# Kernel tuning notes

Hardware: AMD Instinct MI355X
Metric: run time of the kernel (lower is better)

Reference implementation:

```python
import jax, jax.numpy as jnp
import numpy as np

NBITS = 4
DIM = 768
HEADS = 12
HEAD_DIM = DIM // HEADS
B, N = 8, 1024
SCALE = HEAD_DIM ** -0.5


def round_ste(x):
    # round_pass: straight-through round
    return x + jax.lax.stop_gradient(jnp.round(x) - x)


def grad_scale(x, g):
    # forward: x, backward: grad * g
    return x * g + jax.lax.stop_gradient(x * (1.0 - g))


def actq(x, alpha, zp, signed):
    # ActQ eval-mode forward: per-channel alpha/zero_point collapsed via .mean()
    if signed:
        Qn, Qp = -2 ** (NBITS - 1), 2 ** (NBITS - 1) - 1
    else:
        Qn, Qp = 0, 2 ** NBITS - 1
    a = jnp.mean(alpha)
    z = jnp.mean(round_ste(zp))
    xq = round_ste(jnp.clip(x / a + z, Qn, Qp))
    return (xq - z) * a


def linearq(x, w, b, alpha_w, act_alpha, act_zp):
    # LSQ weight quant (per-out-channel alpha with grad_scale) + input ActQ
    Qn, Qp = -2 ** (NBITS - 1), 2 ** (NBITS - 1) - 1
    g = 1.0 / np.sqrt(w.size * Qp)
    a = grad_scale(alpha_w, g)[:, None]  # [out,1]
    w_q = round_ste(jnp.clip(w / a, Qn, Qp)) * a
    xq = actq(x, act_alpha, act_zp, signed=True)
    y = jnp.einsum('...i,oi->...o', xq, w_q)
    return y if b is None else y + b


def layernorm(x, g, b, eps=1e-5):
    m = jnp.mean(x, axis=-1, keepdims=True)
    v = jnp.var(x, axis=-1, keepdims=True)  # biased, matches torch LayerNorm
    return (x - m) / jnp.sqrt(v + eps) * g + b


def setup_inputs() -> dict:
    key = jax.random.key(0)
    ks = jax.random.split(key, 20)
    u = lambda k, shape: jax.random.uniform(k, shape, jnp.float32, 0.01, 0.05)
    zp = lambda k, shape: jax.random.uniform(k, shape, jnp.float32, -0.3, 0.3)
    return {
        'x0': jax.random.normal(ks[0], (B, N, DIM), jnp.float32),
        'qkv_w': jax.random.normal(ks[1], (3 * DIM, DIM), jnp.float32) * 0.02,
        'qkv_alpha_w': u(ks[2], (3 * DIM,)),
        'qkv_act_alpha': u(ks[3], (DIM,)),
        'qkv_act_zp': zp(ks[4], (DIM,)),
        'norm_q_g': jnp.ones((HEAD_DIM,), jnp.float32),
        'norm_q_b': jnp.zeros((HEAD_DIM,), jnp.float32),
        'norm_k_g': jnp.ones((HEAD_DIM,), jnp.float32),
        'norm_k_b': jnp.zeros((HEAD_DIM,), jnp.float32),
        'q_alpha': u(ks[5], (HEADS,)), 'q_zp': zp(ks[6], (HEADS,)),
        'k_alpha': u(ks[7], (HEADS,)), 'k_zp': zp(ks[8], (HEADS,)),
        'v_alpha': u(ks[9], (HEADS,)), 'v_zp': zp(ks[10], (HEADS,)),
        'attn_alpha': u(ks[11], (HEADS,)), 'attn_zp': zp(ks[12], (HEADS,)),
        'proj_w': jax.random.normal(ks[13], (DIM, DIM), jnp.float32) * 0.02,
        'proj_b': jnp.zeros((DIM,), jnp.float32),
        'proj_alpha_w': u(ks[14], (DIM,)),
        'proj_act_alpha': u(ks[15], (DIM,)),
        'proj_act_zp': zp(ks[16], (DIM,)),
    }


def reference(x0, qkv_w, qkv_alpha_w, qkv_act_alpha, qkv_act_zp,
              norm_q_g, norm_q_b, norm_k_g, norm_k_b,
              q_alpha, q_zp, k_alpha, k_zp, v_alpha, v_zp,
              attn_alpha, attn_zp,
              proj_w, proj_b, proj_alpha_w, proj_act_alpha, proj_act_zp):
    b, n, c = x0.shape
    qkv = linearq(x0, qkv_w, None, qkv_alpha_w, qkv_act_alpha, qkv_act_zp)
    qkv = qkv.reshape(b, n, 3, HEADS, HEAD_DIM).transpose(2, 0, 3, 1, 4)  # [3,B,H,N,hd]
    q0, k0, v0 = qkv[0], qkv[1], qkv[2]
    q1 = layernorm(q0, norm_q_g, norm_q_b)
    k1 = layernorm(k0, norm_k_g, norm_k_b)
    q2 = actq(q1, q_alpha, q_zp, signed=True)
    k2 = actq(k1, k_alpha, k_zp, signed=True)
    v2 = actq(v0, v_alpha, v_zp, signed=True)
    attn = jax.nn.softmax(jnp.einsum('bhqd,bhkd->bhqk', q2, k2) * SCALE, axis=-1)
    attn = actq(attn, attn_alpha, attn_zp, signed=False)  # softmax output is unsigned
    x1 = jnp.einsum('bhqk,bhkd->bhqd', attn, v2).transpose(0, 2, 1, 3).reshape(b, n, c)
    return linearq(x1, proj_w, proj_b, proj_alpha_w, proj_act_alpha, proj_act_zp)
```

## Files before the change

### kernel.cpp

```cpp
#include <hip/hip_runtime.h>
#include <hip/hip_bf16.h>

#define HEADS 12
#define HD 64
#define DIM 768
#define SEQ 1024
#define NTOK 8192
#define TRIPLE 2304
#define BHTOT 96

typedef __attribute__((ext_vector_type(8))) short bf16x8;
typedef __attribute__((ext_vector_type(4))) float f32x4;
typedef __attribute__((ext_vector_type(4))) int i32x4;

#define MFMA_B16(a, b, c) __builtin_amdgcn_mfma_f32_16x16x32_bf16((a), (b), (c), 0, 0, 0)
#define MFMA_I8(a, b, c) __builtin_amdgcn_mfma_i32_16x16x64_i8((a), (b), (c), 0, 0, 0)

__device__ __forceinline__ unsigned short f2bf(float f) {
  unsigned int u = __float_as_uint(f);
  unsigned int r = (u + 0x7fffu + ((u >> 16) & 1u)) >> 16;
  return (unsigned short)r;
}
__device__ __forceinline__ float qclamp(float v, float lo, float hi) {
  return fminf(fmaxf(v, lo), hi);
}

__device__ float block_mean(const float* p, int n, int rnd, float* red) {
  int t = threadIdx.x;
  float s = 0.f;
  for (int i = t; i < n; i += 256) { float v = p[i]; s += rnd ? rintf(v) : v; }
  red[t] = s;
  __syncthreads();
  for (int o = 128; o > 0; o >>= 1) { if (t < o) red[t] += red[t + o]; __syncthreads(); }
  float m = red[0] / (float)n;
  __syncthreads();
  return m;
}

__global__ __launch_bounds__(256) void k_prep(
    const float* qaa, const float* qzp, const float* qa, const float* qz,
    const float* ka, const float* kz, const float* va, const float* vz,
    const float* ata, const float* atz, const float* pa, const float* pz,
    float* sc) {
  __shared__ float red[256];
  float r0 = block_mean(qaa, 768, 0, red);
  float r1 = block_mean(qzp, 768, 1, red);
  float r2 = block_mean(qa, 12, 0, red);
  float r3 = block_mean(qz, 12, 1, red);
  float r4 = block_mean(ka, 12, 0, red);
  float r5 = block_mean(kz, 12, 1, red);
  float r6 = block_mean(va, 12, 0, red);
  float r7 = block_mean(vz, 12, 1, red);
  float r8 = block_mean(ata, 12, 0, red);
  float r9 = block_mean(atz, 12, 1, red);
  float r10 = block_mean(pa, 768, 0, red);
  float r11 = block_mean(pz, 768, 1, red);
  if (threadIdx.x == 0) {
    sc[0] = r0; sc[1] = r1; sc[2] = r2; sc[3] = r3; sc[4] = r4; sc[5] = r5;
    sc[6] = r6; sc[7] = r7; sc[8] = r8; sc[9] = r9; sc[10] = r10; sc[11] = r11;
  }
}

__global__ __launch_bounds__(256) void k_quant_act(
    const float* __restrict__ x, signed char* __restrict__ xq,
    const float* __restrict__ sc, int n) {
  int i = (blockIdx.x * 256 + threadIdx.x) * 4;
  if (i >= n) return;
  float a = sc[0], z = sc[1];
  float4 v = *(const float4*)(x + i);
  int b0 = (int)rintf(qclamp(v.x / a + z, -8.f, 7.f));
  int b1 = (int)rintf(qclamp(v.y / a + z, -8.f, 7.f));
  int b2 = (int)rintf(qclamp(v.z / a + z, -8.f, 7.f));
  int b3 = (int)rintf(qclamp(v.w / a + z, -8.f, 7.f));
  ((int*)xq)[i >> 2] = (b0 & 255) | ((b1 & 255) << 8) | ((b2 & 255) << 16) | (b3 << 24);
}

__global__ __launch_bounds__(256) void k_quant_w(
    const float* __restrict__ w, const float* __restrict__ alpha,
    signed char* __restrict__ wq, int n, int K) {
  int i = (blockIdx.x * 256 + threadIdx.x) * 4;
  if (i >= n) return;
  float a = alpha[i / K];
  float4 v = *(const float4*)(w + i);
  int b0 = (int)rintf(qclamp(v.x / a, -8.f, 7.f));
  int b1 = (int)rintf(qclamp(v.y / a, -8.f, 7.f));
  int b2 = (int)rintf(qclamp(v.z / a, -8.f, 7.f));
  int b3 = (int)rintf(qclamp(v.w / a, -8.f, 7.f));
  ((int*)wq)[i >> 2] = (b0 & 255) | ((b1 & 255) << 8) | ((b2 & 255) << 16) | (b3 << 24);
}

__global__ __launch_bounds__(256) void k_wsum(
    const signed char* __restrict__ wq, float* __restrict__ s, int K) {
  const int w = threadIdx.x >> 6, l = threadIdx.x & 63;
  const int row = blockIdx.x * 4 + w;
  const int* rp = (const int*)(wq + (size_t)row * K);
  int acc = 0;
  for (int idx = l; idx < K / 4; idx += 64) {
    int u = rp[idx];
    acc += (int)(signed char)u + (int)(signed char)(u >> 8) +
           (int)(signed char)(u >> 16) + (int)(signed char)(u >> 24);
  }
#pragma unroll
  for (int off = 32; off > 0; off >>= 1) acc += __shfl_xor(acc, off);
  if (l == 0) s[row] = (float)acc;
}

__device__ __forceinline__ void stage_i8(
    const signed char* __restrict__ g, int ldk,
    signed char* lds, int wv, int l) {
#pragma unroll
  for (int j = 0; j < 4; ++j) {
    __builtin_amdgcn_global_load_lds(
        (const __attribute__((address_space(1))) void*)(
            g + (size_t)(wv * 32 + j * 8 + (l >> 3)) * ldk + (l & 7) * 16),
        (__attribute__((address_space(3))) void*)(lds + wv * 4096 + j * 1024),
        16, 0, 0);
  }
}
__device__ __forceinline__ void stage_i8_64(
    const signed char* __restrict__ g, int ldk,
    signed char* lds, int wv, int l) {
#pragma unroll
  for (int j = 0; j < 2; ++j) {
    __builtin_amdgcn_global_load_lds(
        (const __attribute__((address_space(1))) void*)(
            g + (size_t)(wv * 16 + j * 8 + (l >> 3)) * ldk + (l & 7) * 16),
        (__attribute__((address_space(3))) void*)(lds + wv * 2048 + j * 1024),
        16, 0, 0);
  }
}

__global__ __launch_bounds__(256) void k_gemm_qkv(
    const signed char* __restrict__ A, const signed char* __restrict__ Bw,
    const float* __restrict__ colscale, const float* __restrict__ wsum,
    const float* __restrict__ sc,
    const float* __restrict__ nqg, const float* __restrict__ nqb,
    const float* __restrict__ nkg, const float* __restrict__ nkb,
    unsigned short* __restrict__ q2b, unsigned short* __restrict__ k2b,
    unsigned short* __restrict__ v2t) {
  __shared__ __align__(16) char smem[65536];
  signed char (*As)[16384] = (signed char(*)[16384])smem;
  signed char (*Bs)[16384] = (signed char(*)[16384])(smem + 32768);
  unsigned short (*T)[132] = (unsigned short(*)[132])smem;
  const int t = threadIdx.x;
  const int brow = blockIdx.x * 128, bcol = blockIdx.y * 128;
  const int w = t >> 6, l = t & 63;
  const int lr = l & 15, lg = l >> 4;
  const int wr = (w >> 1) * 64, wc = (w & 1) * 64;
  i32x4 acc[4][4] = {};

  auto compute = [&](const signed char* sa, const signed char* sb) {
#pragma unroll
    for (int ks = 0; ks < 2; ++ks) {
      i32x4 af[4], bfr[4];
#pragma unroll
      for (int i = 0; i < 4; ++i) {
        af[i] = *(const i32x4*)&sa[(wr + i * 16 + lr) * 128 + ks * 64 + lg * 16];
        bfr[i] = *(const i32x4*)&sb[(wc + i * 16 + lr) * 128 + ks * 64 + lg * 16];
      }
#pragma unroll
      for (int i = 0; i < 4; ++i)
#pragma unroll
        for (int j = 0; j < 4; ++j)
          acc[i][j] = MFMA_I8(af[i], bfr[j], acc[i][j]);
    }
  };

  const int nt = DIM / 128;
  stage_i8(A + (size_t)brow * DIM, DIM, As[0], w, l);
  stage_i8(Bw + (size_t)bcol * DIM, DIM, Bs[0], w, l);
  __syncthreads();
  int cur = 0;
  for (int kt = 0; kt < nt - 1; ++kt) {
    stage_i8(A + (size_t)brow * DIM + (kt + 1) * 128, DIM, As[cur ^ 1], w, l);
    stage_i8(Bw + (size_t)bcol * DIM + (kt + 1) * 128, DIM, Bs[cur ^ 1], w, l);
    compute(As[cur], Bs[cur]);
    __syncthreads();
    cur ^= 1;
  }
  compute(As[cur], Bs[cur]);

  const float sact = sc[0], zin = sc[1];
  float s_j[4], zw_j[4];
#pragma unroll
  for (int j = 0; j < 4; ++j) {
    const int col = bcol + wc + j * 16 + lr;
    s_j[j] = sact * colscale[col];
    zw_j[j] = zin * wsum[col];
  }
  f32x4 fac[4][4];
#pragma unroll
  for (int i = 0; i < 4; ++i)
#pragma unroll
    for (int j = 0; j < 4; ++j)
#pragma unroll
      for (int r = 0; r < 4; ++r)
        fac[i][j][r] = ((float)acc[i][j][r] - zw_j[j]) * s_j[j];

  const int seg = bcol / DIM;
  const int h0 = ((bcol % DIM) + wc) / 64;
  if (seg < 2) {
    const float* gp = seg ? nkg : nqg;
    const float* bp = seg ? nkb : nqb;
    const float aq_ = seg ? sc[4] : sc[2];
    const float zq_ = seg ? sc[5] : sc[3];
    float gj[4], bj[4];
#pragma unroll
    for (int j = 0; j < 4; ++j) { gj[j] = gp[j * 16 + lr]; bj[j] = bp[j * 16 + lr]; }
    unsigned short* dstb = seg ? k2b : q2b;
#pragma unroll
    for (int i = 0; i < 4; ++i)
#pragma unroll
      for (int r = 0; r < 4; ++r) {
        float sum = fac[i][0][r] + fac[i][1][r] + fac[i][2][r] + fac[i][3][r];
        sum += __shfl_xor(sum, 1); sum += __shfl_xor(sum, 2);
        sum += __shfl_xor(sum, 4); sum += __shfl_xor(sum, 8);
        float m = sum * (1.0f / 64.0f);
        float vs = 0.f;
#pragma unroll
        for (int j = 0; j < 4; ++j) { float d = fac[i][j][r] - m; vs += d * d; }
        vs += __shfl_xor(vs, 1); vs += __shfl_xor(vs, 2);
        vs += __shfl_xor(vs, 4); vs += __shfl_xor(vs, 8);
        float inv = 1.0f / sqrtf(vs * (1.0f / 64.0f) + 1e-5f);
        int row = brow + wr + i * 16 + lg * 4 + r;
        int b_ = row >> 10, n_ = row & (SEQ - 1);
        unsigned short* dst = dstb + (((size_t)(b_ * HEADS + h0) << 10) + n_) * HD;
#pragma unroll
        for (int j = 0; j < 4; ++j) {
          float yv = (fac[i][j][r] - m) * inv * gj[j] + bj[j];
          float qv = rintf(qclamp(yv / aq_ + zq_, -8.f, 7.f)) - zq_;
          dst[j * 16 + lr] = f2bf(qv);
        }
      }
  } else {
    const float av_ = sc[6], zv = sc[7];
    __syncthreads();
#pragma unroll
    for (int i = 0; i < 4; ++i)
#pragma unroll
      for (int r = 0; r < 4; ++r) {
        const int rowl = wr + i * 16 + lg * 4 + r;
#pragma unroll
        for (int j = 0; j < 4; ++j) {
          float qv = rintf(qclamp(fac[i][j][r] / av_ + zv, -8.f, 7.f)) - zv;
          T[wc + j * 16 + lr][rowl] = f2bf(qv);
        }
      }
    __syncthreads();
    const int b_ = brow >> 10, n0 = brow & (SEQ - 1);
    const int hbase = (bcol % DIM) / 64;
#pragma unroll
    for (int it = 0; it < 32; ++it) {
      const int dcol = w * 32 + it;
      const int h_ = hbase + (dcol >> 6);
      const int d_ = dcol & 63;
      unsigned int val = *(const unsigned int*)&T[dcol][2 * l];
      *(unsigned int*)(v2t + ((size_t)(b_ * HEADS + h_) << 16) +
                       (size_t)d_ * SEQ + n0 + 2 * l) = val;
    }
  }
}

__global__ __launch_bounds__(256) void k_gemm(
    const signed char* __restrict__ A, const signed char* __restrict__ Bw,
    float* __restrict__ out, const float* __restrict__ colscale,
    const float* __restrict__ wsum, const float* __restrict__ bias,
    const float* __restrict__ sc, int sact_idx, int zin_idx,
    int M, int Nt, int K) {
  __shared__ signed char As[2][64 * 128];
  __shared__ signed char Bs[2][128 * 128];
  const int t = threadIdx.x;
  const int brow = blockIdx.x * 64, bcol = blockIdx.y * 128;
  const int w = t >> 6, l = t & 63;
  const int lr = l & 15, lg = l >> 4;
  const int wr = (w >> 1) * 32, wc = (w & 1) * 64;
  i32x4 acc[2][4] = {};

  auto compute = [&](const signed char* sa, const signed char* sb) {
#pragma unroll
    for (int ks = 0; ks < 2; ++ks) {
      i32x4 af[2], bfr[4];
#pragma unroll
      for (int i = 0; i < 2; ++i)
        af[i] = *(const i32x4*)&sa[(wr + i * 16 + lr) * 128 + ks * 64 + lg * 16];
#pragma unroll
      for (int j = 0; j < 4; ++j)
        bfr[j] = *(const i32x4*)&sb[(wc + j * 16 + lr) * 128 + ks * 64 + lg * 16];
#pragma unroll
      for (int i = 0; i < 2; ++i)
#pragma unroll
        for (int j = 0; j < 4; ++j)
          acc[i][j] = MFMA_I8(af[i], bfr[j], acc[i][j]);
    }
  };

  const int nt = K / 128;
  stage_i8_64(A + (size_t)brow * K, K, As[0], w, l);
  stage_i8(Bw + (size_t)bcol * K, K, Bs[0], w, l);
  __syncthreads();
  int cur = 0;
  for (int kt = 0; kt < nt - 1; ++kt) {
    stage_i8_64(A + (size_t)brow * K + (kt + 1) * 128, K, As[cur ^ 1], w, l);
    stage_i8(Bw + (size_t)bcol * K + (kt + 1) * 128, K, Bs[cur ^ 1], w, l);
    compute(As[cur], Bs[cur]);
    __syncthreads();
    cur ^= 1;
  }
  compute(As[cur], Bs[cur]);

  const float sact = sc[sact_idx], zin = sc[zin_idx];
#pragma unroll
  for (int j = 0; j < 4; ++j) {
    const int col = bcol + wc + j * 16 + lr;
    const float s = sact * colscale[col];
    const float zw = zin * wsum[col];
    const float bb = bias ? bias[col] : 0.f;
#pragma unroll
    for (int i = 0; i < 2; ++i) {
      const int row0 = brow + wr + i * 16 + lg * 4;
#pragma unroll
      for (int r = 0; r < 4; ++r)
        out[(size_t)(row0 + r) * Nt + col] = ((float)acc[i][j][r] - zw) * s + bb;
    }
  }
}

__global__ __launch_bounds__(256, 3) void k_attn(
    const unsigned short* __restrict__ q2b, const unsigned short* __restrict__ k2b,
    const unsigned short* __restrict__ v2t, signed char* __restrict__ x1q,
    const float* __restrict__ sc) {
  __shared__ unsigned short Ks[128][72];
  __shared__ unsigned short Vs[64][136];
  __shared__ unsigned short Ps[4][32][40];
  const int t = threadIdx.x;
  const int w = t >> 6, l = t & 63;
  const int lr = l & 15, lg = l >> 4;
  const int bid = (int)(blockIdx.x & 7) * 96 + (int)(blockIdx.x >> 3);
  const int bh = bid >> 3, qc = bid & 7;
  const unsigned short* Qg = q2b + (size_t)bh * (SEQ * HD);
  const unsigned short* Kg = k2b + (size_t)bh * (SEQ * HD);
  const unsigned short* Vg = v2t + (size_t)bh * (SEQ * HD);
  const float aq = sc[2], ak = sc[4], av_ = sc[6], aa = sc[8], za = sc[9];
  const float ap = sc[10], zpp = sc[11];
  const float sqk2 = aq * ak * 0.125f * 1.44269504f;
  const float spv = aa * av_;
  const int qr0 = qc * 128 + w * 32;

  bf16x8 qf[2][2];
#pragma unroll
  for (int rt = 0; rt < 2; ++rt)
#pragma unroll
    for (int ks = 0; ks < 2; ++ks)
      qf[rt][ks] = *(const bf16x8*)(Qg + (size_t)(qr0 + rt * 16 + lr) * HD + ks * 32 + lg * 8);

  const int sr = t >> 1, sc0 = (t & 1) * 32;
  const int vr = t >> 2, vc0 = (t & 3) * 32;

  float lacc[2][4] = {};
  for (int kt = 0; kt < SEQ; kt += 128) {
    const uint4* g = (const uint4*)(Kg + (size_t)(kt + sr) * HD + sc0);
    uint4 u0 = g[0], u1 = g[1], u2 = g[2], u3 = g[3];
    __syncthreads();
    { uint4* d = (uint4*)&Ks[sr][sc0]; d[0] = u0; d[1] = u1; d[2] = u2; d[3] = u3; }
    __syncthreads();
#pragma unroll
    for (int ct = 0; ct < 8; ++ct) {
      const int kl = ct * 16 + lr;
      bf16x8 kf0 = *(const bf16x8*)&Ks[kl][lg * 8];
      bf16x8 kf1 = *(const bf16x8*)&Ks[kl][32 + lg * 8];
#pragma unroll
      for (int rt = 0; rt < 2; ++rt) {
        f32x4 s4 = {0.f, 0.f, 0.f, 0.f};
        s4 = MFMA_B16(qf[rt][0], kf0, s4);
        s4 = MFMA_B16(qf[rt][1], kf1, s4);
#pragma unroll
        for (int r = 0; r < 4; ++r)
          lacc[rt][r] += __builtin_amdgcn_exp2f(s4[r] * sqk2);
      }
    }
  }
#pragma unroll
  for (int off = 1; off < 16; off <<= 1)
#pragma unroll
    for (int rt = 0; rt < 2; ++rt)
#pragma unroll
      for (int r = 0; r < 4; ++r) lacc[rt][r] += __shfl_xor(lacc[rt][r], off);
  float pinv[2][4];
#pragma unroll
  for (int rt = 0; rt < 2; ++rt)
#pragma unroll
    for (int r = 0; r < 4; ++r) pinv[rt][r] = 1.0f / (lacc[rt][r] * aa);

  f32x4 oacc[2][4] = {};
  for (int kt = 0; kt < SEQ; kt += 128) {
    const uint4* gk = (const uint4*)(Kg + (size_t)(kt + sr) * HD + sc0);
    uint4 u0 = gk[0], u1 = gk[1], u2 = gk[2], u3 = gk[3];
    const uint4* gv = (const uint4*)(Vg + (size_t)vr * SEQ + kt + vc0);
    uint4 w0 = gv[0], w1 = gv[1], w2 = gv[2], w3 = gv[3];
    __syncthreads();
    { uint4* d = (uint4*)&Ks[sr][sc0]; d[0] = u0; d[1] = u1; d[2] = u2; d[3] = u3; }
    { uint4* d = (uint4*)&Vs[vr][vc0]; d[0] = w0; d[1] = w1; d[2] = w2; d[3] = w3; }
    __syncthreads();
#pragma unroll
    for (int q4 = 0; q4 < 4; ++q4) {
#pragma unroll
      for (int c2 = 0; c2 < 2; ++c2) {
        const int ct = q4 * 2 + c2;
        const int kl = ct * 16 + lr;
        bf16x8 kf0 = *(const bf16x8*)&Ks[kl][lg * 8];
        bf16x8 kf1 = *(const bf16x8*)&Ks[kl][32 + lg * 8];
#pragma unroll
        for (int rt = 0; rt < 2; ++rt) {
          f32x4 s4 = {0.f, 0.f, 0.f, 0.f};
          s4 = MFMA_B16(qf[rt][0], kf0, s4);
          s4 = MFMA_B16(qf[rt][1], kf1, s4);
#pragma unroll
          for (int r = 0; r < 4; ++r) {
            float e = __builtin_amdgcn_exp2f(s4[r] * sqk2);
            float p = fmaf(e, pinv[rt][r], za);
            float qv = rintf(qclamp(p, 0.f, 15.f)) - za;
            Ps[w][rt * 16 + lg * 4 + r][c2 * 16 + lr] = f2bf(qv);
          }
        }
      }
      bf16x8 vf[4], pf[2];
#pragma unroll
      for (int dt = 0; dt < 4; ++dt)
        vf[dt] = *(const bf16x8*)&Vs[dt * 16 + lr][q4 * 32 + lg * 8];
#pragma unroll
      for (int rt = 0; rt < 2; ++rt)
        pf[rt] = *(const bf16x8*)&Ps[w][rt * 16 + lr][lg * 8];
#pragma unroll
      for (int rt = 0; rt < 2; ++rt)
#pragma unroll
        for (int dt = 0; dt < 4; ++dt)
          oacc[rt][dt] = MFMA_B16(pf[rt], vf[dt], oacc[rt][dt]);
    }
  }
  const int b_ = bh / HEADS, h_ = bh % HEADS;
#pragma unroll
  for (int rt = 0; rt < 2; ++rt)
#pragma unroll
    for (int dt = 0; dt < 4; ++dt) {
      const int col = h_ * HD + dt * 16 + lr;
#pragma unroll
      for (int r = 0; r < 4; ++r) {
        const int qrow = qr0 + rt * 16 + lg * 4 + r;
        float x1v = oacc[rt][dt][r] * spv;
        int xi = (int)rintf(qclamp(x1v / ap + zpp, -8.f, 7.f));
        x1q[(size_t)(b_ * SEQ + qrow) * DIM + col] = (signed char)xi;
      }
    }
}

extern "C" void kernel_launch(void* const* d_in, const int* in_sizes, int n_in,
                              void* d_out, int out_size, void* d_ws, size_t ws_size,
                              hipStream_t stream) {
  const float* x0      = (const float*)d_in[0];
  const float* qkvw    = (const float*)d_in[1];
  const float* qkv_aw  = (const float*)d_in[2];
  const float* qkv_aa  = (const float*)d_in[3];
  const float* qkv_azp = (const float*)d_in[4];
  const float* nqg     = (const float*)d_in[5];
  const float* nqb     = (const float*)d_in[6];
  const float* nkg     = (const float*)d_in[7];
  const float* nkb     = (const float*)d_in[8];
  const float* q_a     = (const float*)d_in[9];
  const float* q_z     = (const float*)d_in[10];
  const float* k_a     = (const float*)d_in[11];
  const float* k_z     = (const float*)d_in[12];
  const float* v_a     = (const float*)d_in[13];
  const float* v_z     = (const float*)d_in[14];
  const float* at_a    = (const float*)d_in[15];
  const float* at_z    = (const float*)d_in[16];
  const float* pw      = (const float*)d_in[17];
  const float* pb      = (const float*)d_in[18];
  const float* p_aw    = (const float*)d_in[19];
  const float* p_aa    = (const float*)d_in[20];
  const float* p_azp   = (const float*)d_in[21];
  float* out = (float*)d_out;

  char* ws = (char*)d_ws;
  size_t off = 0;
  float* scal = (float*)(ws); off = 256;
  signed char* x0q  = (signed char*)(ws + off); off += (size_t)NTOK * DIM;
  signed char* qwq  = (signed char*)(ws + off); off += (size_t)TRIPLE * DIM;
  signed char* pwq  = (signed char*)(ws + off); off += (size_t)DIM * DIM;
  float* wsumQ      = (float*)(ws + off);       off += (size_t)TRIPLE * 4;
  float* wsumP      = (float*)(ws + off);       off += (size_t)DIM * 4;
  unsigned short* q2b = (unsigned short*)(ws + off); off += (size_t)BHTOT * SEQ * HD * 2;
  unsigned short* k2b = (unsigned short*)(ws + off); off += (size_t)BHTOT * SEQ * HD * 2;
  unsigned short* v2t = (unsigned short*)(ws + off); off += (size_t)BHTOT * SEQ * HD * 2;
  signed char* x1q  = (signed char*)(ws + off); off += (size_t)NTOK * DIM;

  k_prep<<<1, 256, 0, stream>>>(qkv_aa, qkv_azp, q_a, q_z, k_a, k_z, v_a, v_z,
                                at_a, at_z, p_aa, p_azp, scal);
  k_quant_act<<<(NTOK * DIM) / 1024, 256, 0, stream>>>(x0, x0q, scal, NTOK * DIM);
  k_quant_w<<<(TRIPLE * DIM) / 1024, 256, 0, stream>>>(qkvw, qkv_aw, qwq, TRIPLE * DIM, DIM);
  k_quant_w<<<(DIM * DIM) / 1024, 256, 0, stream>>>(pw, p_aw, pwq, DIM * DIM, DIM);
  k_wsum<<<TRIPLE / 4, 256, 0, stream>>>(qwq, wsumQ, DIM);
  k_wsum<<<DIM / 4, 256, 0, stream>>>(pwq, wsumP, DIM);
  k_gemm_qkv<<<dim3(NTOK / 128, TRIPLE / 128), 256, 0, stream>>>(
      x0q, qwq, qkv_aw, wsumQ, scal, nqg, nqb, nkg, nkb, q2b, k2b, v2t);
  k_attn<<<BHTOT * 8, 256, 0, stream>>>(q2b, k2b, v2t, x1q, scal);
  k_gemm<<<dim3(NTOK / 64, DIM / 128), 256, 0, stream>>>(
      x1q, pwq, out, p_aw, wsumP, pb, scal, 10, 11, NTOK, DIM, DIM);
}
```

Before: 258.9 us.

## Fuse weight quant with row sums, shrink QKV K-tile, narrow proj GEMM tiles

Weight quantization and per-row weight sums are merged into one kernel that quantizes a row and reduces its sum in-wave, dropping two launches and a re-read of the quantized weights. The QKV GEMM moves from a K-tile of 128 to 64, halving LDS use to about 33KB so more blocks can be resident, at the cost of twice as many K iterations and barriers. The projection GEMM switches to 64x64 output tiles, doubling the grid to fill more CUs but lowering per-block data reuse.

Measured after the change: 256.0 us. Within noise of the previous version (-1.1%).

```diff
diff --git a/kernel.cpp b/kernel.cpp
--- a/kernel.cpp
+++ b/kernel.cpp
@@ -75,49 +75,44 @@
   ((int*)xq)[i >> 2] = (b0 & 255) | ((b1 & 255) << 8) | ((b2 & 255) << 16) | (b3 << 24);
 }
 
-__global__ __launch_bounds__(256) void k_quant_w(
+__global__ __launch_bounds__(256) void k_quant_w_ws(
     const float* __restrict__ w, const float* __restrict__ alpha,
-    signed char* __restrict__ wq, int n, int K) {
-  int i = (blockIdx.x * 256 + threadIdx.x) * 4;
-  if (i >= n) return;
-  float a = alpha[i / K];
-  float4 v = *(const float4*)(w + i);
-  int b0 = (int)rintf(qclamp(v.x / a, -8.f, 7.f));
-  int b1 = (int)rintf(qclamp(v.y / a, -8.f, 7.f));
-  int b2 = (int)rintf(qclamp(v.z / a, -8.f, 7.f));
-  int b3 = (int)rintf(qclamp(v.w / a, -8.f, 7.f));
-  ((int*)wq)[i >> 2] = (b0 & 255) | ((b1 & 255) << 8) | ((b2 & 255) << 16) | (b3 << 24);
-}
-
-__global__ __launch_bounds__(256) void k_wsum(
-    const signed char* __restrict__ wq, float* __restrict__ s, int K) {
-  const int w = threadIdx.x >> 6, l = threadIdx.x & 63;
-  const int row = blockIdx.x * 4 + w;
-  const int* rp = (const int*)(wq + (size_t)row * K);
-  int acc = 0;
-  for (int idx = l; idx < K / 4; idx += 64) {
-    int u = rp[idx];
-    acc += (int)(signed char)u + (int)(signed char)(u >> 8) +
-           (int)(signed char)(u >> 16) + (int)(signed char)(u >> 24);
-  }
-#pragma unroll
-  for (int off = 32; off > 0; off >>= 1) acc += __shfl_xor(acc, off);
-  if (l == 0) s[row] = (float)acc;
-}
-
-__device__ __forceinline__ void stage_i8(
+    signed char* __restrict__ wq, float* __restrict__ wsum) {
+  const int wv = threadIdx.x >> 6, l = threadIdx.x & 63;
+  const int row = blockIdx.x * 4 + wv;
+  const float a = alpha[row];
+  const float* src = w + (size_t)row * DIM;
+  int* dst = (int*)(wq + (size_t)row * DIM);
+  int s = 0;
+#pragma unroll
+  for (int j = 0; j < 3; ++j) {
+    const int idx = j * 64 + l;
+    float4 v = *(const float4*)(src + idx * 4);
+    int b0 = (int)rintf(qclamp(v.x / a, -8.f, 7.f));
+    int b1 = (int)rintf(qclamp(v.y / a, -8.f, 7.f));
+    int b2 = (int)rintf(qclamp(v.z / a, -8.f, 7.f));
+    int b3 = (int)rintf(qclamp(v.w / a, -8.f, 7.f));
+    dst[idx] = (b0 & 255) | ((b1 & 255) << 8) | ((b2 & 255) << 16) | (b3 << 24);
+    s += b0 + b1 + b2 + b3;
+  }
+#pragma unroll
+  for (int off = 32; off > 0; off >>= 1) s += __shfl_xor(s, off);
+  if (l == 0) wsum[row] = (float)s;
+}
+
+__device__ __forceinline__ void stage128x64_i8(
     const signed char* __restrict__ g, int ldk,
     signed char* lds, int wv, int l) {
 #pragma unroll
-  for (int j = 0; j < 4; ++j) {
+  for (int j = 0; j < 2; ++j) {
     __builtin_amdgcn_global_load_lds(
         (const __attribute__((address_space(1))) void*)(
-            g + (size_t)(wv * 32 + j * 8 + (l >> 3)) * ldk + (l & 7) * 16),
-        (__attribute__((address_space(3))) void*)(lds + wv * 4096 + j * 1024),
+            g + (size_t)(wv * 32 + j * 16 + (l >> 2)) * ldk + (l & 3) * 16),
+        (__attribute__((address_space(3))) void*)(lds + wv * 2048 + j * 1024),
         16, 0, 0);
   }
 }
-__device__ __forceinline__ void stage_i8_64(
+__device__ __forceinline__ void stage64x128_i8(
     const signed char* __restrict__ g, int ldk,
     signed char* lds, int wv, int l) {
 #pragma unroll
@@ -138,9 +133,9 @@
     const float* __restrict__ nkg, const float* __restrict__ nkb,
     unsigned short* __restrict__ q2b, unsigned short* __restrict__ k2b,
     unsigned short* __restrict__ v2t) {
-  __shared__ __align__(16) char smem[65536];
-  signed char (*As)[16384] = (signed char(*)[16384])smem;
-  signed char (*Bs)[16384] = (signed char(*)[16384])(smem + 32768);
+  __shared__ __align__(16) char smem[33792];
+  signed char (*As)[8192] = (signed char(*)[8192])smem;
+  signed char (*Bs)[8192] = (signed char(*)[8192])(smem + 16384);
   unsigned short (*T)[132] = (unsigned short(*)[132])smem;
   const int t = threadIdx.x;
   const int brow = blockIdx.x * 128, bcol = blockIdx.y * 128;
@@ -150,30 +145,27 @@
   i32x4 acc[4][4] = {};
 
   auto compute = [&](const signed char* sa, const signed char* sb) {
-#pragma unroll
-    for (int ks = 0; ks < 2; ++ks) {
-      i32x4 af[4], bfr[4];
-#pragma unroll
-      for (int i = 0; i < 4; ++i) {
-        af[i] = *(const i32x4*)&sa[(wr + i * 16 + lr) * 128 + ks * 64 + lg * 16];
-        bfr[i] = *(const i32x4*)&sb[(wc + i * 16 + lr) * 128 + ks * 64 + lg * 16];
-      }
-#pragma unroll
-      for (int i = 0; i < 4; ++i)
-#pragma unroll
-        for (int j = 0; j < 4; ++j)
-          acc[i][j] = MFMA_I8(af[i], bfr[j], acc[i][j]);
-    }
+    i32x4 af[4], bfr[4];
+#pragma unroll
+    for (int i = 0; i < 4; ++i) {
+      af[i] = *(const i32x4*)&sa[(wr + i * 16 + lr) * 64 + lg * 16];
+      bfr[i] = *(const i32x4*)&sb[(wc + i * 16 + lr) * 64 + lg * 16];
+    }
+#pragma unroll
+    for (int i = 0; i < 4; ++i)
+#pragma unroll
+      for (int j = 0; j < 4; ++j)
+        acc[i][j] = MFMA_I8(af[i], bfr[j], acc[i][j]);
   };
 
-  const int nt = DIM / 128;
-  stage_i8(A + (size_t)brow * DIM, DIM, As[0], w, l);
-  stage_i8(Bw + (size_t)bcol * DIM, DIM, Bs[0], w, l);
+  const int nt = DIM / 64;
+  stage128x64_i8(A + (size_t)brow * DIM, DIM, As[0], w, l);
+  stage128x64_i8(Bw + (size_t)bcol * DIM, DIM, Bs[0], w, l);
   __syncthreads();
   int cur = 0;
   for (int kt = 0; kt < nt - 1; ++kt) {
-    stage_i8(A + (size_t)brow * DIM + (kt + 1) * 128, DIM, As[cur ^ 1], w, l);
-    stage_i8(Bw + (size_t)bcol * DIM + (kt + 1) * 128, DIM, Bs[cur ^ 1], w, l);
+    stage128x64_i8(A + (size_t)brow * DIM + (kt + 1) * 64, DIM, As[cur ^ 1], w, l);
+    stage128x64_i8(Bw + (size_t)bcol * DIM + (kt + 1) * 64, DIM, Bs[cur ^ 1], w, l);
     compute(As[cur], Bs[cur]);
     __syncthreads();
     cur ^= 1;
@@ -268,40 +260,39 @@
     const float* __restrict__ sc, int sact_idx, int zin_idx,
     int M, int Nt, int K) {
   __shared__ signed char As[2][64 * 128];
-  __shared__ signed char Bs[2][128 * 128];
+  __shared__ signed char Bs[2][64 * 128];
   const int t = threadIdx.x;
-  const int brow = blockIdx.x * 64, bcol = blockIdx.y * 128;
+  const int brow = blockIdx.x * 64, bcol = blockIdx.y * 64;
   const int w = t >> 6, l = t & 63;
   const int lr = l & 15, lg = l >> 4;
-  const int wr = (w >> 1) * 32, wc = (w & 1) * 64;
-  i32x4 acc[2][4] = {};
+  const int wr = (w >> 1) * 32, wc = (w & 1) * 32;
+  i32x4 acc[2][2] = {};
 
   auto compute = [&](const signed char* sa, const signed char* sb) {
 #pragma unroll
     for (int ks = 0; ks < 2; ++ks) {
-      i32x4 af[2], bfr[4];
+      i32x4 af[2], bfr[2];
+#pragma unroll
+      for (int i = 0; i < 2; ++i) {
+        af[i] = *(const i32x4*)&sa[(wr + i * 16 + lr) * 128 + ks * 64 + lg * 16];
+        bfr[i] = *(const i32x4*)&sb[(wc + i * 16 + lr) * 128 + ks * 64 + lg * 16];
+      }
 #pragma unroll
       for (int i = 0; i < 2; ++i)
-        af[i] = *(const i32x4*)&sa[(wr + i * 16 + lr) * 128 + ks * 64 + lg * 16];
-#pragma unroll
-      for (int j = 0; j < 4; ++j)
-        bfr[j] = *(const i32x4*)&sb[(wc + j * 16 + lr) * 128 + ks * 64 + lg * 16];
-#pragma unroll
-      for (int i = 0; i < 2; ++i)
-#pragma unroll
-        for (int j = 0; j < 4; ++j)
+#pragma unroll
+        for (int j = 0; j < 2; ++j)
           acc[i][j] = MFMA_I8(af[i], bfr[j], acc[i][j]);
     }
   };
 
   const int nt = K / 128;
-  stage_i8_64(A + (size_t)brow * K, K, As[0], w, l);
-  stage_i8(Bw + (size_t)bcol * K, K, Bs[0], w, l);
+  stage64x128_i8(A + (size_t)brow * K, K, As[0], w, l);
+  stage64x128_i8(Bw + (size_t)bcol * K, K, Bs[0], w, l);
   __syncthreads();
   int cur = 0;
   for (int kt = 0; kt < nt - 1; ++kt) {
-    stage_i8_64(A + (size_t)brow * K + (kt + 1) * 128, K, As[cur ^ 1], w, l);
-    stage_i8(Bw + (size_t)bcol * K + (kt + 1) * 128, K, Bs[cur ^ 1], w, l);
+    stage64x128_i8(A + (size_t)brow * K + (kt + 1) * 128, K, As[cur ^ 1], w, l);
+    stage64x128_i8(Bw + (size_t)bcol * K + (kt + 1) * 128, K, Bs[cur ^ 1], w, l);
     compute(As[cur], Bs[cur]);
     __syncthreads();
     cur ^= 1;
@@ -310,7 +301,7 @@
 
   const float sact = sc[sact_idx], zin = sc[zin_idx];
 #pragma unroll
-  for (int j = 0; j < 4; ++j) {
+  for (int j = 0; j < 2; ++j) {
     const int col = bcol + wc + j * 16 + lr;
     const float s = sact * colscale[col];
     const float zw = zin * wsum[col];
@@ -496,13 +487,11 @@
   k_prep<<<1, 256, 0, stream>>>(qkv_aa, qkv_azp, q_a, q_z, k_a, k_z, v_a, v_z,
                                 at_a, at_z, p_aa, p_azp, scal);
   k_quant_act<<<(NTOK * DIM) / 1024, 256, 0, stream>>>(x0, x0q, scal, NTOK * DIM);
-  k_quant_w<<<(TRIPLE * DIM) / 1024, 256, 0, stream>>>(qkvw, qkv_aw, qwq, TRIPLE * DIM, DIM);
-  k_quant_w<<<(DIM * DIM) / 1024, 256, 0, stream>>>(pw, p_aw, pwq, DIM * DIM, DIM);
-  k_wsum<<<TRIPLE / 4, 256, 0, stream>>>(qwq, wsumQ, DIM);
-  k_wsum<<<DIM / 4, 256, 0, stream>>>(pwq, wsumP, DIM);
+  k_quant_w_ws<<<TRIPLE / 4, 256, 0, stream>>>(qkvw, qkv_aw, qwq, wsumQ);
+  k_quant_w_ws<<<DIM / 4, 256, 0, stream>>>(pw, p_aw, pwq, wsumP);
   k_gemm_qkv<<<dim3(NTOK / 128, TRIPLE / 128), 256, 0, stream>>>(
       x0q, qwq, qkv_aw, wsumQ, scal, nqg, nqb, nkg, nkb, q2b, k2b, v2t);
   k_attn<<<BHTOT * 8, 256, 0, stream>>>(q2b, k2b, v2t, x1q, scal);
-  k_gemm<<<dim3(NTOK / 64, DIM / 128), 256, 0, stream>>>(
+  k_gemm<<<dim3(NTOK / 64, DIM / 64), 256, 0, stream>>>(
       x1q, pwq, out, p_aw, wsumP, pb, scal, 10, 11, NTOK, DIM, DIM);
 }
```
